# Kernel tuning notes

Hardware: AMD Instinct MI355X
Metric: run time of the kernel (lower is better)

## Reference

```python
import jax, jax.numpy as jnp
import numpy as np

B, NPG, D, E = 64, 1024, 128, 524288
N = B * NPG
K1, K2, K3 = 820, 656, 525  # ceil(0.8*1024), ceil(0.8*820), ceil(0.8*656)
VOCAB = 100000
EPS = 1e-5


def setup_inputs() -> dict:
    key = jax.random.key(0)
    ks = jax.random.split(key, 16)
    epg = E // B
    off = jnp.repeat(jnp.arange(B, dtype=jnp.int32) * NPG, epg)
    src = jax.random.randint(ks[0], (E,), 0, NPG, dtype=jnp.int32) + off
    dst = jax.random.randint(ks[1], (E,), 0, NPG, dtype=jnp.int32) + off
    edge_index = jnp.stack([src, dst])  # [2, E], within-graph edges
    node_idx = jax.random.randint(ks[2], (N, 1), 0, VOCAB, dtype=jnp.int32)
    def lin(k, o, i):
        return jax.random.normal(k, (o, i), jnp.float32) / np.sqrt(i).astype(np.float32)
    return dict(
        node_idx=node_idx, edge_index=edge_index,
        emb=jax.random.normal(ks[3], (VOCAB, D), jnp.float32),
        w1l=lin(ks[4], 128, D), b1l=jnp.zeros(128, jnp.float32), w1r=lin(ks[5], 128, D),
        pool_w=jax.random.normal(ks[6], (128,), jnp.float32) / np.float32(np.sqrt(128)),
        w2l=lin(ks[7], 128, 128), b2l=jnp.zeros(128, jnp.float32), w2r=lin(ks[8], 128, 128),
        fc1_w=lin(ks[9], 128, 256), fc1_b=jnp.zeros(128, jnp.float32),
        bn1_g=jnp.ones(128, jnp.float32), bn1_b=jnp.zeros(128, jnp.float32),
        fc2_w=lin(ks[10], 64, 128), fc2_b=jnp.zeros(64, jnp.float32),
        bn2_g=jnp.ones(64, jnp.float32), bn2_b=jnp.zeros(64, jnp.float32),
        lin_w=lin(ks[11], 1, 64), lin_b=jnp.zeros(1, jnp.float32),
    )


def _sage(x, src, dst, em, wl, bl, wr):
    # PyG SAGEConv: lin_l(mean_{j->i} x_j) + lin_r(x_i); em masks dropped edges
    n = x.shape[0]
    s = jax.ops.segment_sum(x[src] * em[:, None], dst, num_segments=n)
    c = jax.ops.segment_sum(em, dst, num_segments=n)
    mean = s / jnp.maximum(c, 1.0)[:, None]
    return mean @ wl.T + bl + x @ wr.T


def _topk(x, src, dst, em, w, k):
    # PyG TopKPooling: score = x.w/||w||, per-graph top-k, gate by tanh(score)
    n = x.shape[0]
    npg = n // B
    score = (x @ w) / jnp.linalg.norm(w)
    vals, idx = jax.lax.top_k(score.reshape(B, npg), k)  # [B,k]
    perm = (idx + (jnp.arange(B, dtype=idx.dtype) * npg)[:, None]).reshape(-1)
    xn = x[perm] * jnp.tanh(vals).reshape(-1)[:, None]
    new_id = jnp.full((n,), -1, jnp.int32).at[perm].set(jnp.arange(B * k, dtype=jnp.int32))
    ns, nd = new_id[src], new_id[dst]
    em2 = em * (ns >= 0) * (nd >= 0)  # keep only edges with both endpoints kept
    return xn, jnp.maximum(ns, 0), jnp.maximum(nd, 0), em2


def _readout(x, k):
    # global_max_pool || global_mean_pool (graphs are contiguous, size k)
    xr = x.reshape(B, k, -1)
    return jnp.concatenate([xr.max(axis=1), xr.mean(axis=1)], axis=1)


def _bn(x, g, b):
    m = x.mean(0)
    v = jnp.mean((x - m) ** 2, axis=0)  # biased var, as in BatchNorm1d training
    return (x - m) / jnp.sqrt(v + EPS) * g + b


def reference(node_idx, edge_index, emb, w1l, b1l, w1r, pool_w,
              w2l, b2l, w2r, fc1_w, fc1_b, bn1_g, bn1_b,
              fc2_w, fc2_b, bn2_g, bn2_b, lin_w, lin_b):
    src, dst = edge_index[0], edge_index[1]
    em = jnp.ones((E,), jnp.float32)
    x = emb[node_idx[:, 0]]                                   # [N,128]
    x = jax.nn.relu(_sage(x, src, dst, em, w1l, b1l, w1r))
    x, src, dst, em = _topk(x, src, dst, em, pool_w, K1)
    x1 = _readout(x, K1)
    x = jax.nn.relu(_sage(x, src, dst, em, w2l, b2l, w2r))
    x, src, dst, em = _topk(x, src, dst, em, pool_w, K2)
    x2 = _readout(x, K2)
    x = jax.nn.relu(_sage(x, src, dst, em, w2l, b2l, w2r))
    x, src, dst, em = _topk(x, src, dst, em, pool_w, K3)
    x3 = _readout(x, K3)
    h = x1 + x2 + x3                                          # [B,256]
    h = jax.nn.relu(_bn(h @ fc1_w.T + fc1_b, bn1_g, bn1_b))
    h = jax.nn.relu(_bn(h @ fc2_w.T + fc2_b, bn2_g, bn2_b))
    # dropout is identity in eval mode
    return jax.nn.sigmoid(h @ lin_w.T + lin_b)[:, 0]          # [B]
```

## Files before the change

### kernel.cpp

```cpp
#include <hip/hip_runtime.h>
#include <hip/hip_bf16.h>
#include <cstdint>
#include <cstddef>

#define NGRAPH 64
#define NPG0   1024
#define NNODE  65536
#define NEDGE  524288
#define EPG    8192
#define DIM    128
#define RCHUNK 16
#define PSTRIDE ((size_t)NGRAPH * RCHUNK * 128)
#define AROWS  32

typedef __attribute__((ext_vector_type(8))) short short8v;
typedef __attribute__((ext_vector_type(4))) float f32x4;

__device__ __forceinline__ unsigned bf16rne(float f) {
  unsigned u = __float_as_uint(f);
  return (u + 0x7FFFu + ((u >> 16) & 1u)) >> 16;
}

__device__ __forceinline__ void drain_row(const int* __restrict__ el,
    const float* __restrict__ x, int l32, int e, int end, float4& acc)
{
  for (; e + 4 <= end; e += 4) {
    int s0 = el[e], s1 = el[e+1], s2 = el[e+2], s3 = el[e+3];
    float4 a0 = ((const float4*)(x + (size_t)s0 * DIM))[l32];
    float4 a1 = ((const float4*)(x + (size_t)s1 * DIM))[l32];
    float4 a2 = ((const float4*)(x + (size_t)s2 * DIM))[l32];
    float4 a3 = ((const float4*)(x + (size_t)s3 * DIM))[l32];
    acc.x += (a0.x + a1.x) + (a2.x + a3.x);
    acc.y += (a0.y + a1.y) + (a2.y + a3.y);
    acc.z += (a0.z + a1.z) + (a2.z + a3.z);
    acc.w += (a0.w + a1.w) + (a2.w + a3.w);
  }
  for (; e < end; ++e) {
    float4 a = ((const float4*)(x + (size_t)el[e] * DIM))[l32];
    acc.x += a.x; acc.y += a.y; acc.z += a.z; acc.w += a.w;
  }
}

__global__ __launch_bounds__(256) void k_gather(const float* __restrict__ emb,
    const int* __restrict__ nid, float* __restrict__ x)
{
  int tid = blockIdx.x * 256 + threadIdx.x;
  int i = tid >> 5, lane = tid & 31;
  int row = nid[i];
  ((float4*)(x + (size_t)i * DIM))[lane] =
      ((const float4*)(emb + (size_t)row * DIM))[lane];
}

__global__ __launch_bounds__(64) void k_norm(const float* __restrict__ pw,
    float* __restrict__ inv_norm)
{
  int t = threadIdx.x;
  float a = pw[t], b = pw[t + 64];
  float v = a * a + b * b;
  for (int off = 32; off; off >>= 1) v += __shfl_xor(v, off);
  if (t == 0) *inv_norm = 1.0f / sqrtf(v);
}

__global__ __launch_bounds__(256) void k_prep_wfrag(
    const float* __restrict__ w1l, const float* __restrict__ w1r,
    const float* __restrict__ w2l, const float* __restrict__ w2r,
    short* __restrict__ whiF, short* __restrict__ wloF)
{
  int id = blockIdx.x * 256 + threadIdx.x;
  int set = id >> 15;
  int r = id & 32767;
  int j  = r & 7;
  int l  = (r >> 3) & 63;
  int nt = (r >> 9) & 7;
  int kk = r >> 12;
  int k = kk * 32 + ((l >> 4) & 3) * 8 + j;
  int n = nt * 16 + (l & 15);
  const float* wl = set ? w2l : w1l;
  const float* wr = set ? w2r : w1r;
  float w = (k < 128) ? wl[n * 128 + k] : wr[n * 128 + (k - 128)];
  unsigned hb = bf16rne(w);
  float hif = __uint_as_float(hb << 16);
  unsigned lb = bf16rne(w - hif);
  whiF[id] = (short)hb;
  wloF[id] = (short)lb;
}

__global__ __launch_bounds__(1024) void k_csr0(const int* __restrict__ ei,
    int* __restrict__ off_g, int* __restrict__ elist_g, float* __restrict__ c_out)
{
  __shared__ int cnt[1024];
  __shared__ int cur[1024];
  __shared__ int wsum[16];
  const int t = threadIdx.x, g = blockIdx.x;
  const int nodeBase = g * NPG0;
  const int e0 = g * EPG;
  cnt[t] = 0;
  __syncthreads();
  int sv8[8], dl8[8];
  #pragma unroll
  for (int i = 0; i < 8; ++i) {
    int e = e0 + t + i * 1024;
    sv8[i] = ei[e];
    dl8[i] = ei[NEDGE + e] - nodeBase;
    atomicAdd(&cnt[dl8[i]], 1);
  }
  __syncthreads();
  const int lane = t & 63, w = t >> 6;
  int cv = cnt[t];
  int x = cv;
  #pragma unroll
  for (int off = 1; off < 64; off <<= 1) {
    int y = __shfl_up(x, off);
    if (lane >= off) x += y;
  }
  if (lane == 63) wsum[w] = x;
  __syncthreads();
  if (t < 16) {
    int v = wsum[t];
    #pragma unroll
    for (int off2 = 1; off2 < 16; off2 <<= 1) {
      int y = __shfl_up(v, off2);
      if (t >= off2) v += y;
    }
    wsum[t] = v;
  }
  __syncthreads();
  int incl = x + (w ? wsum[w - 1] : 0);
  int excl = incl - cv;
  cur[t] = excl;
  int* offp = off_g + g * 1025;
  offp[t] = excl;
  if (t == 1023) offp[1024] = incl;
  c_out[nodeBase + t] = (float)cv;
  __syncthreads();
  int* elp = elist_g + g * EPG;
  #pragma unroll
  for (int i = 0; i < 8; ++i) {
    int pos = atomicAdd(&cur[dl8[i]], 1);
    elp[pos] = sv8[i];
  }
}

__global__ __launch_bounds__(128) void k_agg_gemm(
    const int* __restrict__ off_g, const int* __restrict__ elist_g,
    const float* __restrict__ x, float* __restrict__ h_out,
    const short* __restrict__ whiF, const short* __restrict__ wloF,
    const float* __restrict__ bl, const float* __restrict__ pw,
    float* __restrict__ score, int npg)
{
  __shared__ float sA[AROWS * 128];
  __shared__ float cntA[AROWS];
  const int g     = blockIdx.x & 63;
  const int slice = blockIdx.x >> 6;
  const int nodeBase = g * npg;
  const int vbase = slice * AROWS;
  const int t = threadIdx.x;
  float4* sA4 = (float4*)sA;

  {
    const int gr = t >> 5, l32 = t & 31;
    const int* off = off_g + g * 1025;
    const int* el  = elist_g + g * EPG;
    #pragma unroll
    for (int ip = 0; ip < 4; ++ip) {
      const int vbA = gr * 8 + ip * 2, vbB = vbA + 1;
      const int vA = vbase + vbA, vB = vbase + vbB;
      float4 accA = {0.f,0.f,0.f,0.f}, accB = {0.f,0.f,0.f,0.f};
      int eA = 0, endA = 0, eB = 0, endB = 0;
      if (vA < npg) { eA = off[vA]; endA = off[vA + 1]; }
      if (vB < npg) { eB = off[vB]; endB = off[vB + 1]; }
      const int cnA = endA - eA, cnB = endB - eB;
      while (eA + 4 <= endA && eB + 4 <= endB) {
        int a0 = el[eA], a1 = el[eA+1], a2 = el[eA+2], a3 = el[eA+3];
        int b0 = el[eB], b1 = el[eB+1], b2 = el[eB+2], b3 = el[eB+3];
        float4 xa0 = ((const float4*)(x + (size_t)a0 * DIM))[l32];
        float4 xa1 = ((const float4*)(x + (size_t)a1 * DIM))[l32];
        float4 xa2 = ((const float4*)(x + (size_t)a2 * DIM))[l32];
        float4 xa3 = ((const float4*)(x + (size_t)a3 * DIM))[l32];
        float4 xb0 = ((const float4*)(x + (size_t)b0 * DIM))[l32];
        float4 xb1 = ((const float4*)(x + (size_t)b1 * DIM))[l32];
        float4 xb2 = ((const float4*)(x + (size_t)b2 * DIM))[l32];
        float4 xb3 = ((const float4*)(x + (size_t)b3 * DIM))[l32];
        accA.x += (xa0.x + xa1.x) + (xa2.x + xa3.x);
        accA.y += (xa0.y + xa1.y) + (xa2.y + xa3.y);
        accA.z += (xa0.z + xa1.z) + (xa2.z + xa3.z);
        accA.w += (xa0.w + xa1.w) + (xa2.w + xa3.w);
        accB.x += (xb0.x + xb1.x) + (xb2.x + xb3.x);
        accB.y += (xb0.y + xb1.y) + (xb2.y + xb3.y);
        accB.z += (xb0.z + xb1.z) + (xb2.z + xb3.z);
        accB.w += (xb0.w + xb1.w) + (xb2.w + xb3.w);
        eA += 4; eB += 4;
      }
      drain_row(el, x, l32, eA, endA, accA);
      drain_row(el, x, l32, eB, endB, accB);
      sA4[vbA * 32 + (l32 ^ (vbA & 7))] = accA;
      sA4[vbB * 32 + (l32 ^ (vbB & 7))] = accB;
      if (l32 == 0) { cntA[vbA] = (float)cnA; cntA[vbB] = (float)cnB; }
    }
  }
  __syncthreads();

  const int wv = t >> 6, l = t & 63;
  const int lrow = l & 15, lk = l >> 4;
  const int rb = wv * 16;
  const int rowb = rb + lrow;
  const int rsw = rowb & 7;
  const int rowg = nodeBase + min(vbase + rowb, npg - 1);
  const float invc = 1.0f / fmaxf(cntA[rowb], 1.0f);
  f32x4 acc[8];
  #pragma unroll
  for (int nt = 0; nt < 8; ++nt) acc[nt] = (f32x4){0.f, 0.f, 0.f, 0.f};
  const float4* sArow = sA4 + rowb * 32;
  const float* xrow = x + (size_t)rowg * DIM + lk * 8;
  const short8v* bh = (const short8v*)whiF;
  const short8v* bo = (const short8v*)wloF;

  #pragma unroll
  for (int kk = 0; kk < 8; ++kk) {
    float av[8];
    if (kk < 4) {
      int sbase = kk * 8 + lk * 2;
      float4 a0 = sArow[(sbase + 0) ^ rsw];
      float4 a1 = sArow[(sbase + 1) ^ rsw];
      av[0] = a0.x * invc; av[1] = a0.y * invc;
      av[2] = a0.z * invc; av[3] = a0.w * invc;
      av[4] = a1.x * invc; av[5] = a1.y * invc;
      av[6] = a1.z * invc; av[7] = a1.w * invc;
    } else {
      float4 a0 = *(const float4*)(xrow + (kk - 4) * 32);
      float4 a1 = *(const float4*)(xrow + (kk - 4) * 32 + 4);
      av[0] = a0.x; av[1] = a0.y; av[2] = a0.z; av[3] = a0.w;
      av[4] = a1.x; av[5] = a1.y; av[6] = a1.z; av[7] = a1.w;
    }
    short8v ahi, alo;
    #pragma unroll
    for (int j = 0; j < 8; ++j) {
      unsigned hb = bf16rne(av[j]);
      float hif = __uint_as_float(hb << 16);
      ahi[j] = (short)hb;
      alo[j] = (short)bf16rne(av[j] - hif);
    }
    #pragma unroll
    for (int nt = 0; nt < 8; ++nt) {
      int fi = (kk * 8 + nt) * 64 + l;
      short8v bhi = bh[fi];
      short8v blo = bo[fi];
      acc[nt] = __builtin_amdgcn_mfma_f32_16x16x32_bf16(ahi, bhi, acc[nt], 0, 0, 0);
      acc[nt] = __builtin_amdgcn_mfma_f32_16x16x32_bf16(alo, bhi, acc[nt], 0, 0, 0);
      acc[nt] = __builtin_amdgcn_mfma_f32_16x16x32_bf16(ahi, blo, acc[nt], 0, 0, 0);
    }
  }

  float sp0 = 0.f, sp1 = 0.f, sp2 = 0.f, sp3 = 0.f;
  const int mbv = vbase + rb + lk * 4;
  #pragma unroll
  for (int nt = 0; nt < 8; ++nt) {
    int col = nt * 16 + lrow;
    float bb = bl[col], pv = pw[col];
    float h0 = fmaxf(acc[nt][0] + bb, 0.f);
    float h1 = fmaxf(acc[nt][1] + bb, 0.f);
    float h2 = fmaxf(acc[nt][2] + bb, 0.f);
    float h3 = fmaxf(acc[nt][3] + bb, 0.f);
    if (mbv + 0 < npg) h_out[(size_t)(nodeBase + mbv + 0) * DIM + col] = h0;
    if (mbv + 1 < npg) h_out[(size_t)(nodeBase + mbv + 1) * DIM + col] = h1;
    if (mbv + 2 < npg) h_out[(size_t)(nodeBase + mbv + 2) * DIM + col] = h2;
    if (mbv + 3 < npg) h_out[(size_t)(nodeBase + mbv + 3) * DIM + col] = h3;
    sp0 += h0 * pv; sp1 += h1 * pv; sp2 += h2 * pv; sp3 += h3 * pv;
  }
  #pragma unroll
  for (int off = 1; off <= 8; off <<= 1) {
    sp0 += __shfl_xor(sp0, off);
    sp1 += __shfl_xor(sp1, off);
    sp2 += __shfl_xor(sp2, off);
    sp3 += __shfl_xor(sp3, off);
  }
  if (lrow == 0) {
    if (mbv + 0 < npg) score[nodeBase + mbv + 0] = sp0;
    if (mbv + 1 < npg) score[nodeBase + mbv + 1] = sp1;
    if (mbv + 2 < npg) score[nodeBase + mbv + 2] = sp2;
    if (mbv + 3 < npg) score[nodeBase + mbv + 3] = sp3;
  }
}

__global__ __launch_bounds__(1024) void k_topk_fused(
    const float* __restrict__ score, const float* __restrict__ inv_norm_p,
    int npg, int k, int* __restrict__ sel_pos, float* __restrict__ sel_scale,
    int build_next, int write_eout,
    const int* __restrict__ ein_src, const int* __restrict__ ein_dst,
    int* __restrict__ eout_src, int* __restrict__ eout_dst,
    int* __restrict__ off_g, int* __restrict__ elist_g, float* __restrict__ c_out)
{
  __shared__ float key[1024];
  __shared__ int   idxs[1024];
  __shared__ int   nid[1024];
  __shared__ int   cnt[1024];
  __shared__ int   cur[1024];
  __shared__ int   wsum[16];
  const int t = threadIdx.x, g = blockIdx.x;
  const int base = g * npg;
  float rk = (t < npg) ? score[base + t] : -3.402823466e38f;
  int   ri = t;
  nid[t] = -1;
  cnt[t] = 0;

  #pragma unroll
  for (int size = 2; size <= 1024; size <<= 1) {
    for (int stride = size >> 1; stride >= 64; stride >>= 1) {
      key[t] = rk; idxs[t] = ri;
      __syncthreads();
      float km = key[t ^ stride];
      int   im = idxs[t ^ stride];
      __syncthreads();
      bool mf = (rk > km) || (rk == km && ri < im);
      bool desc = ((t & size) == 0);
      bool lower = ((t & stride) == 0);
      bool keep = desc ? (lower ? mf : !mf) : (lower ? !mf : mf);
      if (!keep) { rk = km; ri = im; }
    }
    for (int stride = (size >> 1) > 32 ? 32 : (size >> 1); stride >= 1; stride >>= 1) {
      float km = __shfl_xor(rk, stride);
      int   im = __shfl_xor(ri, stride);
      bool mf = (rk > km) || (rk == km && ri < im);
      bool desc = ((t & size) == 0);
      bool lower = ((t & stride) == 0);
      bool keep = desc ? (lower ? mf : !mf) : (lower ? !mf : mf);
      if (!keep) { rk = km; ri = im; }
    }
  }

  if (t < k) {
    float inv = *inv_norm_p;
    nid[ri] = t;
    sel_pos[g * k + t] = base + ri;
    sel_scale[g * k + t] = tanhf(rk * inv);
  }
  if (!build_next) return;
  __syncthreads();
  const int e0 = g * EPG;
  const int newBase = g * k;
  int lns[8], lnd[8];
  #pragma unroll
  for (int i = 0; i < 8; ++i) {
    int e = e0 + t + i * 1024;
    int sv = ein_src[e];
    int ns = -1, nd = -1;
    if (sv >= 0) {
      int dv = ein_dst[e];
      ns = nid[sv - base];
      nd = nid[dv - base];
      if (ns < 0 || nd < 0) ns = -1;
    }
    lns[i] = ns; lnd[i] = nd;
    if (write_eout) {
      eout_src[e] = (ns >= 0) ? (newBase + ns) : -1;
      eout_dst[e] = (ns >= 0) ? (newBase + nd) : -1;
    }
    if (ns >= 0) atomicAdd(&cnt[nd], 1);
  }
  __syncthreads();
  const int lane = t & 63, w = t >> 6;
  int cv = cnt[t];
  int x = cv;
  #pragma unroll
  for (int off = 1; off < 64; off <<= 1) {
    int y = __shfl_up(x, off);
    if (lane >= off) x += y;
  }
  if (lane == 63) wsum[w] = x;
  __syncthreads();
  if (t < 16) {
    int v = wsum[t];
    #pragma unroll
    for (int off2 = 1; off2 < 16; off2 <<= 1) {
      int y = __shfl_up(v, off2);
      if (t >= off2) v += y;
    }
    wsum[t] = v;
  }
  __syncthreads();
  int incl = x + (w ? wsum[w - 1] : 0);
  int excl = incl - cv;
  cur[t] = excl;
  off_g[g * 1025 + t] = excl;
  if (t < k) c_out[newBase + t] = (float)cv;
  __syncthreads();
  int* elp = elist_g + g * EPG;
  #pragma unroll
  for (int i = 0; i < 8; ++i) {
    if (lns[i] >= 0) {
      int pos = atomicAdd(&cur[lnd[i]], 1);
      elp[pos] = newBase + lns[i];
    }
  }
}

__global__ __launch_bounds__(256) void k_pool_part(const float* __restrict__ h,
    const int* __restrict__ sel_pos, const float* __restrict__ sel_scale, int k,
    float* __restrict__ xo, float* __restrict__ pmax, float* __restrict__ psum)
{
  __shared__ float4 smx[256], ssm[256];
  const int b  = blockIdx.x >> 4;
  const int ch = blockIdx.x & (RCHUNK - 1);
  const int rpc = (k + RCHUNK - 1) / RCHUNK;
  const int r0 = ch * rpc;
  const int r1 = min(k, r0 + rpc);
  const int d4  = threadIdx.x & 31;
  const int sub = threadIdx.x >> 5;
  const float NEG = -3.402823466e38f;
  float4 mx = {NEG, NEG, NEG, NEG};
  float4 sm = {0.f, 0.f, 0.f, 0.f};
  for (int r = r0 + sub; r < r1; r += 8) {
    int j = b * k + r;
    float scv = sel_scale[j];
    float4 v = ((const float4*)(h + (size_t)sel_pos[j] * DIM))[d4];
    v.x *= scv; v.y *= scv; v.z *= scv; v.w *= scv;
    ((float4*)(xo + (size_t)j * DIM))[d4] = v;
    mx.x = fmaxf(mx.x, v.x); mx.y = fmaxf(mx.y, v.y);
    mx.z = fmaxf(mx.z, v.z); mx.w = fmaxf(mx.w, v.w);
    sm.x += v.x; sm.y += v.y; sm.z += v.z; sm.w += v.w;
  }
  smx[threadIdx.x] = mx; ssm[threadIdx.x] = sm;
  __syncthreads();
  if (sub < 4) {
    #pragma unroll
    for (int step = 4; step >= 1; step >>= 1) {
      if (sub < step) {
        float4 m2 = smx[(sub + step) * 32 + d4];
        float4 s2 = ssm[(sub + step) * 32 + d4];
        mx = smx[sub * 32 + d4]; sm = ssm[sub * 32 + d4];
        mx.x = fmaxf(mx.x, m2.x); mx.y = fmaxf(mx.y, m2.y);
        mx.z = fmaxf(mx.z, m2.z); mx.w = fmaxf(mx.w, m2.w);
        sm.x += s2.x; sm.y += s2.y; sm.z += s2.z; sm.w += s2.w;
        smx[sub * 32 + d4] = mx; ssm[sub * 32 + d4] = sm;
      }
      __syncthreads();
    }
  }
  if (sub == 0) {
    int o = (b * RCHUNK + ch) * 32 + d4;
    ((float4*)pmax)[o] = smx[d4];
    ((float4*)psum)[o] = ssm[d4];
  }
}

__global__ __launch_bounds__(128) void k_readout_final3(
    const float* __restrict__ pmax, const float* __restrict__ psum,
    int k0, int k1, int k2, float* __restrict__ rdT)
{
  int b = blockIdx.x, d = threadIdx.x;
  const int ks[3] = {k0, k1, k2};
  float tmx = 0.f, tmn = 0.f;
  #pragma unroll
  for (int s = 0; s < 3; ++s) {
    const float* pm = pmax + (size_t)s * PSTRIDE;
    const float* ps = psum + (size_t)s * PSTRIDE;
    float mx = -3.402823466e38f, sm = 0.f;
    #pragma unroll
    for (int c = 0; c < RCHUNK; ++c) {
      int o = (b * RCHUNK + c) * 128 + d;
      mx = fmaxf(mx, pm[o]);
      sm += ps[o];
    }
    tmx += mx;
    tmn += sm / (float)ks[s];
  }
  rdT[d * 64 + b] = tmx;
  rdT[(128 + d) * 64 + b] = tmn;
}

__global__ __launch_bounds__(512) void k_mlp_fc1(const float* __restrict__ rdT,
    const float* __restrict__ fc1_w, const float* __restrict__ fc1_b,
    const float* __restrict__ g1, const float* __restrict__ be1,
    float* __restrict__ y1n)
{
  __shared__ float W[8 * 256];
  __shared__ float R[256 * 64];
  const int t = threadIdx.x, b = blockIdx.x;
  ((float4*)W)[t] = ((const float4*)(fc1_w + (size_t)b * 8 * 256))[t];
  #pragma unroll
  for (int i = 0; i < 8; ++i)
    ((float4*)R)[t + i * 512] = ((const float4*)rdT)[t + i * 512];
  __syncthreads();
  const int g = t & 63, w = t >> 6;
  const float* wrow = W + w * 256;
  float acc = 0.f;
  #pragma unroll 4
  for (int k = 0; k < 256; ++k) acc += R[k * 64 + g] * wrow[k];
  int f = b * 8 + w;
  float y = acc + fc1_b[f];
  float s = y, s2 = y * y;
  #pragma unroll
  for (int off = 32; off; off >>= 1) {
    s  += __shfl_xor(s,  off);
    s2 += __shfl_xor(s2, off);
  }
  float mu = s * 0.015625f;
  float var = s2 * 0.015625f - mu * mu;
  float inv = 1.0f / sqrtf(var + 1e-5f);
  y1n[f * 64 + g] = fmaxf((y - mu) * inv * g1[f] + be1[f], 0.f);
}

__global__ __launch_bounds__(1024) void k_mlp_rest(const float* __restrict__ y1n,
    const float* __restrict__ fc2_w, const float* __restrict__ fc2_b,
    const float* __restrict__ g2, const float* __restrict__ be2,
    const float* __restrict__ lin_w, const float* __restrict__ lin_b,
    float* __restrict__ out)
{
  __shared__ float W2[64 * 128];
  __shared__ float Y[128 * 64];
  __shared__ float part[16 * 64];
  const int t = threadIdx.x;
  #pragma unroll
  for (int i = 0; i < 2; ++i) {
    ((float4*)W2)[t + i * 1024] = ((const float4*)fc2_w)[t + i * 1024];
    ((float4*)Y) [t + i * 1024] = ((const float4*)y1n)[t + i * 1024];
  }
  __syncthreads();
  const int g = t & 63, w = t >> 6;
  float acc2[4] = {0.f, 0.f, 0.f, 0.f};
  const float* w20 = W2 + (w * 4 + 0) * 128;
  const float* w21 = W2 + (w * 4 + 1) * 128;
  const float* w22 = W2 + (w * 4 + 2) * 128;
  const float* w23 = W2 + (w * 4 + 3) * 128;
  #pragma unroll 4
  for (int k = 0; k < 128; ++k) {
    float yv = Y[k * 64 + g];
    acc2[0] += yv * w20[k];
    acc2[1] += yv * w21[k];
    acc2[2] += yv * w22[k];
    acc2[3] += yv * w23[k];
  }
  float pp = 0.f;
  #pragma unroll
  for (int j = 0; j < 4; ++j) {
    int m = w * 4 + j;
    float y = acc2[j] + fc2_b[m];
    float s = y, s2 = y * y;
    #pragma unroll
    for (int off = 32; off; off >>= 1) {
      s  += __shfl_xor(s,  off);
      s2 += __shfl_xor(s2, off);
    }
    float mu = s * 0.015625f;
    float var = s2 * 0.015625f - mu * mu;
    float inv = 1.0f / sqrtf(var + 1e-5f);
    float yn = fmaxf((y - mu) * inv * g2[m] + be2[m], 0.f);
    pp += yn * lin_w[m];
  }
  part[w * 64 + g] = pp;
  __syncthreads();
  if (w == 0) {
    float a = lin_b[0];
    #pragma unroll
    for (int c = 0; c < 16; ++c) a += part[c * 64 + g];
    out[g] = 1.0f / (1.0f + expf(-a));
  }
}

extern "C" void kernel_launch(void* const* d_in, const int* in_sizes, int n_in,
                              void* d_out, int out_size, void* d_ws, size_t ws_size,
                              hipStream_t stream) {
  const int*   node_idx = (const int*)  d_in[0];
  const int*   edge_idx = (const int*)  d_in[1];
  const float* emb      = (const float*)d_in[2];
  const float* w1l      = (const float*)d_in[3];
  const float* b1l      = (const float*)d_in[4];
  const float* w1r      = (const float*)d_in[5];
  const float* pool_w   = (const float*)d_in[6];
  const float* w2l      = (const float*)d_in[7];
  const float* b2l      = (const float*)d_in[8];
  const float* w2r      = (const float*)d_in[9];
  const float* fc1_w    = (const float*)d_in[10];
  const float* fc1_b    = (const float*)d_in[11];
  const float* bn1_g    = (const float*)d_in[12];
  const float* bn1_b    = (const float*)d_in[13];
  const float* fc2_w    = (const float*)d_in[14];
  const float* fc2_b    = (const float*)d_in[15];
  const float* bn2_g    = (const float*)d_in[16];
  const float* bn2_b    = (const float*)d_in[17];
  const float* lin_w    = (const float*)d_in[18];
  const float* lin_b    = (const float*)d_in[19];
  float* out = (float*)d_out;

  char* p = (char*)d_ws;
  auto alloc = [&](size_t bytes) -> void* {
    void* r = (void*)p;
    p += (bytes + 255) & ~(size_t)255;
    return r;
  };
  float* x_cur     = (float*)alloc((size_t)NNODE * DIM * 4);
  float* s_buf     = (float*)alloc((size_t)NNODE * DIM * 4);
  float* c_buf     = (float*)alloc((size_t)NNODE * 4);
  float* score     = (float*)alloc((size_t)NNODE * 4);
  int*   sel_pos   = (int*)  alloc((size_t)NGRAPH * 820 * 4);
  float* sel_scale = (float*)alloc((size_t)NGRAPH * 820 * 4);
  int*   src_cur   = (int*)  alloc((size_t)NEDGE * 4);
  int*   dst_cur   = (int*)  alloc((size_t)NEDGE * 4);
  int*   off_g     = (int*)  alloc((size_t)NGRAPH * 1025 * 4);
  int*   elist_g   = (int*)  alloc((size_t)NGRAPH * EPG * 4);
  float* rdT       = (float*)alloc((size_t)256 * 64 * 4);
  short* whiF      = (short*)alloc((size_t)2 * 32768 * 2);
  short* wloF      = (short*)alloc((size_t)2 * 32768 * 2);
  float* y1n       = (float*)alloc((size_t)128 * 64 * 4);
  float* pmax      = (float*)alloc(PSTRIDE * 3 * 4);
  float* psum      = (float*)alloc(PSTRIDE * 3 * 4);
  float* inv_norm  = (float*)alloc(256);

  k_gather<<<NNODE * 32 / 256, 256, 0, stream>>>(emb, node_idx, x_cur);
  k_norm<<<1, 64, 0, stream>>>(pool_w, inv_norm);
  k_prep_wfrag<<<256, 256, 0, stream>>>(w1l, w1r, w2l, w2r, whiF, wloF);
  k_csr0<<<NGRAPH, 1024, 0, stream>>>(edge_idx, off_g, elist_g, c_buf);

  const int Ks[3] = {820, 656, 525};
  int npg = NPG0;
  for (int stage = 0; stage < 3; ++stage) {
    const short* whi_s = whiF + (stage ? 32768 : 0);
    const short* wlo_s = wloF + (stage ? 32768 : 0);
    const float* bl    = stage ? b2l : b1l;
    int k = Ks[stage];
    int slices = (npg + AROWS - 1) / AROWS;

    k_agg_gemm<<<slices * 64, 128, 0, stream>>>(off_g, elist_g, x_cur, s_buf,
                                                whi_s, wlo_s, bl, pool_w,
                                                score, npg);
    const int* ein_s = (stage == 0) ? edge_idx          : src_cur;
    const int* ein_d = (stage == 0) ? (edge_idx + NEDGE) : dst_cur;
    k_topk_fused<<<NGRAPH, 1024, 0, stream>>>(score, inv_norm, npg, k,
        sel_pos, sel_scale,
        (stage < 2) ? 1 : 0, (stage == 0) ? 1 : 0,
        ein_s, ein_d, src_cur, dst_cur,
        off_g, elist_g, c_buf);
    k_pool_part<<<NGRAPH * RCHUNK, 256, 0, stream>>>(s_buf, sel_pos, sel_scale, k,
        x_cur, pmax + (size_t)stage * PSTRIDE, psum + (size_t)stage * PSTRIDE);
    npg = k;
  }

  k_readout_final3<<<NGRAPH, 128, 0, stream>>>(pmax, psum, Ks[0], Ks[1], Ks[2], rdT);
  k_mlp_fc1<<<16, 512, 0, stream>>>(rdT, fc1_w, fc1_b, bn1_g, bn1_b, y1n);
  k_mlp_rest<<<1, 1024, 0, stream>>>(y1n, fc2_w, fc2_b, bn2_g, bn2_b,
                                     lin_w, lin_b, out);
}
```

Before: 264.6 us.

## Store node features in bf16 to halve gather traffic and drop MFMA

Node feature and hidden activation buffers change from fp32 to bf16 across the gather, aggregation-GEMM and pooling kernels. This halves the bytes moved by the random neighbour gathers and the per-stage writes and reads. Because self features are now exactly bf16, their low-part MFMA term is skipped. The cost is lower precision: intermediate activations are rounded to bf16, which may shift top-k selections and the final outputs relative to the fp32 reference.

```diff
diff --git a/kernel.cpp b/kernel.cpp
--- a/kernel.cpp
+++ b/kernel.cpp
@@ -20,35 +20,44 @@
   unsigned u = __float_as_uint(f);
   return (u + 0x7FFFu + ((u >> 16) & 1u)) >> 16;
 }
+__device__ __forceinline__ unsigned pack2bf(float a, float b) {
+  return bf16rne(a) | (bf16rne(b) << 16);
+}
+__device__ __forceinline__ float bf_lo(unsigned u) { return __uint_as_float(u << 16); }
+__device__ __forceinline__ float bf_hi(unsigned u) { return __uint_as_float(u & 0xffff0000u); }
 
 __device__ __forceinline__ void drain_row(const int* __restrict__ el,
-    const float* __restrict__ x, int l32, int e, int end, float4& acc)
+    const uint2* __restrict__ xb, int l32, int e, int end, float4& acc)
 {
   for (; e + 4 <= end; e += 4) {
     int s0 = el[e], s1 = el[e+1], s2 = el[e+2], s3 = el[e+3];
-    float4 a0 = ((const float4*)(x + (size_t)s0 * DIM))[l32];
-    float4 a1 = ((const float4*)(x + (size_t)s1 * DIM))[l32];
-    float4 a2 = ((const float4*)(x + (size_t)s2 * DIM))[l32];
-    float4 a3 = ((const float4*)(x + (size_t)s3 * DIM))[l32];
-    acc.x += (a0.x + a1.x) + (a2.x + a3.x);
-    acc.y += (a0.y + a1.y) + (a2.y + a3.y);
-    acc.z += (a0.z + a1.z) + (a2.z + a3.z);
-    acc.w += (a0.w + a1.w) + (a2.w + a3.w);
+    uint2 a0 = xb[(size_t)s0 * 32 + l32];
+    uint2 a1 = xb[(size_t)s1 * 32 + l32];
+    uint2 a2 = xb[(size_t)s2 * 32 + l32];
+    uint2 a3 = xb[(size_t)s3 * 32 + l32];
+    acc.x += (bf_lo(a0.x) + bf_lo(a1.x)) + (bf_lo(a2.x) + bf_lo(a3.x));
+    acc.y += (bf_hi(a0.x) + bf_hi(a1.x)) + (bf_hi(a2.x) + bf_hi(a3.x));
+    acc.z += (bf_lo(a0.y) + bf_lo(a1.y)) + (bf_lo(a2.y) + bf_lo(a3.y));
+    acc.w += (bf_hi(a0.y) + bf_hi(a1.y)) + (bf_hi(a2.y) + bf_hi(a3.y));
   }
   for (; e < end; ++e) {
-    float4 a = ((const float4*)(x + (size_t)el[e] * DIM))[l32];
-    acc.x += a.x; acc.y += a.y; acc.z += a.z; acc.w += a.w;
+    uint2 a = xb[(size_t)el[e] * 32 + l32];
+    acc.x += bf_lo(a.x); acc.y += bf_hi(a.x);
+    acc.z += bf_lo(a.y); acc.w += bf_hi(a.y);
   }
 }
 
 __global__ __launch_bounds__(256) void k_gather(const float* __restrict__ emb,
-    const int* __restrict__ nid, float* __restrict__ x)
+    const int* __restrict__ nid, unsigned short* __restrict__ xbf)
 {
   int tid = blockIdx.x * 256 + threadIdx.x;
   int i = tid >> 5, lane = tid & 31;
   int row = nid[i];
-  ((float4*)(x + (size_t)i * DIM))[lane] =
-      ((const float4*)(emb + (size_t)row * DIM))[lane];
+  float4 v = ((const float4*)(emb + (size_t)row * DIM))[lane];
+  uint2 u;
+  u.x = pack2bf(v.x, v.y);
+  u.y = pack2bf(v.z, v.w);
+  ((uint2*)xbf)[(size_t)i * 32 + lane] = u;
 }
 
 __global__ __launch_bounds__(64) void k_norm(const float* __restrict__ pw,
@@ -143,7 +152,7 @@
 
 __global__ __launch_bounds__(128) void k_agg_gemm(
     const int* __restrict__ off_g, const int* __restrict__ elist_g,
-    const float* __restrict__ x, float* __restrict__ h_out,
+    const unsigned short* __restrict__ xbf, unsigned short* __restrict__ hbf,
     const short* __restrict__ whiF, const short* __restrict__ wloF,
     const float* __restrict__ bl, const float* __restrict__ pw,
     float* __restrict__ score, int npg)
@@ -156,6 +165,7 @@
   const int vbase = slice * AROWS;
   const int t = threadIdx.x;
   float4* sA4 = (float4*)sA;
+  const uint2* xb2 = (const uint2*)xbf;
 
   {
     const int gr = t >> 5, l32 = t & 31;
@@ -173,26 +183,26 @@
       while (eA + 4 <= endA && eB + 4 <= endB) {
         int a0 = el[eA], a1 = el[eA+1], a2 = el[eA+2], a3 = el[eA+3];
         int b0 = el[eB], b1 = el[eB+1], b2 = el[eB+2], b3 = el[eB+3];
-        float4 xa0 = ((const float4*)(x + (size_t)a0 * DIM))[l32];
-        float4 xa1 = ((const float4*)(x + (size_t)a1 * DIM))[l32];
-        float4 xa2 = ((const float4*)(x + (size_t)a2 * DIM))[l32];
-        float4 xa3 = ((const float4*)(x + (size_t)a3 * DIM))[l32];
-        float4 xb0 = ((const float4*)(x + (size_t)b0 * DIM))[l32];
-        float4 xb1 = ((const float4*)(x + (size_t)b1 * DIM))[l32];
-        float4 xb2 = ((const float4*)(x + (size_t)b2 * DIM))[l32];
-        float4 xb3 = ((const float4*)(x + (size_t)b3 * DIM))[l32];
-        accA.x += (xa0.x + xa1.x) + (xa2.x + xa3.x);
-        accA.y += (xa0.y + xa1.y) + (xa2.y + xa3.y);
-        accA.z += (xa0.z + xa1.z) + (xa2.z + xa3.z);
-        accA.w += (xa0.w + xa1.w) + (xa2.w + xa3.w);
-        accB.x += (xb0.x + xb1.x) + (xb2.x + xb3.x);
-        accB.y += (xb0.y + xb1.y) + (xb2.y + xb3.y);
-        accB.z += (xb0.z + xb1.z) + (xb2.z + xb3.z);
-        accB.w += (xb0.w + xb1.w) + (xb2.w + xb3.w);
+        uint2 xa0 = xb2[(size_t)a0 * 32 + l32];
+        uint2 xa1 = xb2[(size_t)a1 * 32 + l32];
+        uint2 xa2 = xb2[(size_t)a2 * 32 + l32];
+        uint2 xa3 = xb2[(size_t)a3 * 32 + l32];
+        uint2 xb0 = xb2[(size_t)b0 * 32 + l32];
+        uint2 xb1 = xb2[(size_t)b1 * 32 + l32];
+        uint2 xv2 = xb2[(size_t)b2 * 32 + l32];
+        uint2 xv3 = xb2[(size_t)b3 * 32 + l32];
+        accA.x += (bf_lo(xa0.x) + bf_lo(xa1.x)) + (bf_lo(xa2.x) + bf_lo(xa3.x));
+        accA.y += (bf_hi(xa0.x) + bf_hi(xa1.x)) + (bf_hi(xa2.x) + bf_hi(xa3.x));
+        accA.z += (bf_lo(xa0.y) + bf_lo(xa1.y)) + (bf_lo(xa2.y) + bf_lo(xa3.y));
+        accA.w += (bf_hi(xa0.y) + bf_hi(xa1.y)) + (bf_hi(xa2.y) + bf_hi(xa3.y));
+        accB.x += (bf_lo(xb0.x) + bf_lo(xb1.x)) + (bf_lo(xv2.x) + bf_lo(xv3.x));
+        accB.y += (bf_hi(xb0.x) + bf_hi(xb1.x)) + (bf_hi(xv2.x) + bf_hi(xv3.x));
+        accB.z += (bf_lo(xb0.y) + bf_lo(xb1.y)) + (bf_lo(xv2.y) + bf_lo(xv3.y));
+        accB.w += (bf_hi(xb0.y) + bf_hi(xb1.y)) + (bf_hi(xv2.y) + bf_hi(xv3.y));
         eA += 4; eB += 4;
       }
-      drain_row(el, x, l32, eA, endA, accA);
-      drain_row(el, x, l32, eB, endB, accB);
+      drain_row(el, xb2, l32, eA, endA, accA);
+      drain_row(el, xb2, l32, eB, endB, accB);
       sA4[vbA * 32 + (l32 ^ (vbA & 7))] = accA;
       sA4[vbB * 32 + (l32 ^ (vbB & 7))] = accB;
       if (l32 == 0) { cntA[vbA] = (float)cnA; cntA[vbB] = (float)cnB; }
@@ -211,34 +221,33 @@
   #pragma unroll
   for (int nt = 0; nt < 8; ++nt) acc[nt] = (f32x4){0.f, 0.f, 0.f, 0.f};
   const float4* sArow = sA4 + rowb * 32;
-  const float* xrow = x + (size_t)rowg * DIM + lk * 8;
+  const uint4* xrow4 = (const uint4*)xbf + (size_t)rowg * 16;
   const short8v* bh = (const short8v*)whiF;
   const short8v* bo = (const short8v*)wloF;
 
   #pragma unroll
   for (int kk = 0; kk < 8; ++kk) {
-    float av[8];
-    if (kk < 4) {
+    short8v ahi, alo;
+    bool self16 = (kk >= 4);
+    if (!self16) {
       int sbase = kk * 8 + lk * 2;
       float4 a0 = sArow[(sbase + 0) ^ rsw];
       float4 a1 = sArow[(sbase + 1) ^ rsw];
-      av[0] = a0.x * invc; av[1] = a0.y * invc;
-      av[2] = a0.z * invc; av[3] = a0.w * invc;
-      av[4] = a1.x * invc; av[5] = a1.y * invc;
-      av[6] = a1.z * invc; av[7] = a1.w * invc;
+      float av[8] = { a0.x * invc, a0.y * invc, a0.z * invc, a0.w * invc,
+                      a1.x * invc, a1.y * invc, a1.z * invc, a1.w * invc };
+      #pragma unroll
+      for (int j = 0; j < 8; ++j) {
+        unsigned hb2 = bf16rne(av[j]);
+        float hif = __uint_as_float(hb2 << 16);
+        ahi[j] = (short)hb2;
+        alo[j] = (short)bf16rne(av[j] - hif);
+      }
     } else {
-      float4 a0 = *(const float4*)(xrow + (kk - 4) * 32);
-      float4 a1 = *(const float4*)(xrow + (kk - 4) * 32 + 4);
-      av[0] = a0.x; av[1] = a0.y; av[2] = a0.z; av[3] = a0.w;
-      av[4] = a1.x; av[5] = a1.y; av[6] = a1.z; av[7] = a1.w;
-    }
-    short8v ahi, alo;
-    #pragma unroll
-    for (int j = 0; j < 8; ++j) {
-      unsigned hb = bf16rne(av[j]);
-      float hif = __uint_as_float(hb << 16);
-      ahi[j] = (short)hb;
-      alo[j] = (short)bf16rne(av[j] - hif);
+      uint4 u = xrow4[(kk - 4) * 4 + lk];
+      ahi[0] = (short)(u.x & 0xffff); ahi[1] = (short)(u.x >> 16);
+      ahi[2] = (short)(u.y & 0xffff); ahi[3] = (short)(u.y >> 16);
+      ahi[4] = (short)(u.z & 0xffff); ahi[5] = (short)(u.z >> 16);
+      ahi[6] = (short)(u.w & 0xffff); ahi[7] = (short)(u.w >> 16);
     }
     #pragma unroll
     for (int nt = 0; nt < 8; ++nt) {
@@ -246,7 +255,8 @@
       short8v bhi = bh[fi];
       short8v blo = bo[fi];
       acc[nt] = __builtin_amdgcn_mfma_f32_16x16x32_bf16(ahi, bhi, acc[nt], 0, 0, 0);
-      acc[nt] = __builtin_amdgcn_mfma_f32_16x16x32_bf16(alo, bhi, acc[nt], 0, 0, 0);
+      if (!self16)
+        acc[nt] = __builtin_amdgcn_mfma_f32_16x16x32_bf16(alo, bhi, acc[nt], 0, 0, 0);
       acc[nt] = __builtin_amdgcn_mfma_f32_16x16x32_bf16(ahi, blo, acc[nt], 0, 0, 0);
     }
   }
@@ -261,10 +271,10 @@
     float h1 = fmaxf(acc[nt][1] + bb, 0.f);
     float h2 = fmaxf(acc[nt][2] + bb, 0.f);
     float h3 = fmaxf(acc[nt][3] + bb, 0.f);
-    if (mbv + 0 < npg) h_out[(size_t)(nodeBase + mbv + 0) * DIM + col] = h0;
-    if (mbv + 1 < npg) h_out[(size_t)(nodeBase + mbv + 1) * DIM + col] = h1;
-    if (mbv + 2 < npg) h_out[(size_t)(nodeBase + mbv + 2) * DIM + col] = h2;
-    if (mbv + 3 < npg) h_out[(size_t)(nodeBase + mbv + 3) * DIM + col] = h3;
+    if (mbv + 0 < npg) hbf[(size_t)(nodeBase + mbv + 0) * DIM + col] = (unsigned short)bf16rne(h0);
+    if (mbv + 1 < npg) hbf[(size_t)(nodeBase + mbv + 1) * DIM + col] = (unsigned short)bf16rne(h1);
+    if (mbv + 2 < npg) hbf[(size_t)(nodeBase + mbv + 2) * DIM + col] = (unsigned short)bf16rne(h2);
+    if (mbv + 3 < npg) hbf[(size_t)(nodeBase + mbv + 3) * DIM + col] = (unsigned short)bf16rne(h3);
     sp0 += h0 * pv; sp1 += h1 * pv; sp2 += h2 * pv; sp3 += h3 * pv;
   }
   #pragma unroll
@@ -394,9 +404,9 @@
   }
 }
 
-__global__ __launch_bounds__(256) void k_pool_part(const float* __restrict__ h,
+__global__ __launch_bounds__(256) void k_pool_part(const unsigned short* __restrict__ hbf,
     const int* __restrict__ sel_pos, const float* __restrict__ sel_scale, int k,
-    float* __restrict__ xo, float* __restrict__ pmax, float* __restrict__ psum)
+    unsigned short* __restrict__ xbf, float* __restrict__ pmax, float* __restrict__ psum)
 {
   __shared__ float4 smx[256], ssm[256];
   const int b  = blockIdx.x >> 4;
@@ -407,14 +417,22 @@
   const int d4  = threadIdx.x & 31;
   const int sub = threadIdx.x >> 5;
   const float NEG = -3.402823466e38f;
+  const uint2* hb2 = (const uint2*)hbf;
+  uint2* xb2 = (uint2*)xbf;
   float4 mx = {NEG, NEG, NEG, NEG};
   float4 sm = {0.f, 0.f, 0.f, 0.f};
   for (int r = r0 + sub; r < r1; r += 8) {
     int j = b * k + r;
     float scv = sel_scale[j];
-    float4 v = ((const float4*)(h + (size_t)sel_pos[j] * DIM))[d4];
-    v.x *= scv; v.y *= scv; v.z *= scv; v.w *= scv;
-    ((float4*)(xo + (size_t)j * DIM))[d4] = v;
+    uint2 u = hb2[(size_t)sel_pos[j] * 32 + d4];
+    float4 v;
+    v.x = bf_lo(u.x) * scv; v.y = bf_hi(u.x) * scv;
+    v.z = bf_lo(u.y) * scv; v.w = bf_hi(u.y) * scv;
+    uint2 o;
+    o.x = pack2bf(v.x, v.y);
+    o.y = pack2bf(v.z, v.w);
+    xb2[(size_t)j * 32 + d4] = o;
+    v.x = bf_lo(o.x); v.y = bf_hi(o.x); v.z = bf_lo(o.y); v.w = bf_hi(o.y);
     mx.x = fmaxf(mx.x, v.x); mx.y = fmaxf(mx.y, v.y);
     mx.z = fmaxf(mx.z, v.z); mx.w = fmaxf(mx.w, v.w);
     sm.x += v.x; sm.y += v.y; sm.z += v.z; sm.w += v.w;
@@ -588,8 +606,8 @@
     p += (bytes + 255) & ~(size_t)255;
     return r;
   };
-  float* x_cur     = (float*)alloc((size_t)NNODE * DIM * 4);
-  float* s_buf     = (float*)alloc((size_t)NNODE * DIM * 4);
+  unsigned short* x_bf = (unsigned short*)alloc((size_t)NNODE * DIM * 2);
+  unsigned short* h_bf = (unsigned short*)alloc((size_t)NNODE * DIM * 2);
   float* c_buf     = (float*)alloc((size_t)NNODE * 4);
   float* score     = (float*)alloc((size_t)NNODE * 4);
   int*   sel_pos   = (int*)  alloc((size_t)NGRAPH * 820 * 4);
@@ -606,7 +624,7 @@
   float* psum      = (float*)alloc(PSTRIDE * 3 * 4);
   float* inv_norm  = (float*)alloc(256);
 
-  k_gather<<<NNODE * 32 / 256, 256, 0, stream>>>(emb, node_idx, x_cur);
+  k_gather<<<NNODE * 32 / 256, 256, 0, stream>>>(emb, node_idx, x_bf);
   k_norm<<<1, 64, 0, stream>>>(pool_w, inv_norm);
   k_prep_wfrag<<<256, 256, 0, stream>>>(w1l, w1r, w2l, w2r, whiF, wloF);
   k_csr0<<<NGRAPH, 1024, 0, stream>>>(edge_idx, off_g, elist_g, c_buf);
@@ -620,7 +638,7 @@
     int k = Ks[stage];
     int slices = (npg + AROWS - 1) / AROWS;
 
-    k_agg_gemm<<<slices * 64, 128, 0, stream>>>(off_g, elist_g, x_cur, s_buf,
+    k_agg_gemm<<<slices * 64, 128, 0, stream>>>(off_g, elist_g, x_bf, h_bf,
                                                 whi_s, wlo_s, bl, pool_w,
                                                 score, npg);
     const int* ein_s = (stage == 0) ? edge_idx          : src_cur;
@@ -630,8 +648,8 @@
         (stage < 2) ? 1 : 0, (stage == 0) ? 1 : 0,
         ein_s, ein_d, src_cur, dst_cur,
         off_g, elist_g, c_buf);
-    k_pool_part<<<NGRAPH * RCHUNK, 256, 0, stream>>>(s_buf, sel_pos, sel_scale, k,
-        x_cur, pmax + (size_t)stage * PSTRIDE, psum + (size_t)stage * PSTRIDE);
+    k_pool_part<<<NGRAPH * RCHUNK, 256, 0, stream>>>(h_bf, sel_pos, sel_scale, k,
+        x_bf, pmax + (size_t)stage * PSTRIDE, psum + (size_t)stage * PSTRIDE);
     npg = k;
   }
 
```

Result: faster. 251.4 us (-5.0%).
